# Performance work log

Measured on AMD Instinct MI355X. Metric: run time of the kernel, lower is better.

## Reference

```python
import jax, jax.numpy as jnp
import numpy as np

B, H, S, D_K = 4, 16, 2048, 64


def setup_inputs() -> dict:
    key = jax.random.key(0)
    kq, kk, kv = jax.random.split(key, 3)
    Q = jax.random.normal(kq, (B, H, S, D_K), dtype=jnp.float32)
    K = jax.random.normal(kk, (B, H, S, D_K), dtype=jnp.float32)
    V = jax.random.normal(kv, (B, H, S, D_K), dtype=jnp.float32)
    # causal mask: True = masked (matches torch masked_fill_ semantics)
    attn_mask = jnp.triu(jnp.ones((S, S), dtype=jnp.bool_), k=1)[None, None]
    return {"Q": Q, "K": K, "V": V, "attn_mask": attn_mask}


def reference(Q, K, V, attn_mask):
    d_k = Q.shape[-1]
    scale = 1.0 / np.sqrt(d_k).astype(np.float32)
    # scores: [B,H,S,S]
    scores = jnp.einsum("bhqd,bhkd->bhqk", Q, K) * scale
    scores = jnp.where(attn_mask, jnp.float32(-1e9), scores)
    attn = jax.nn.softmax(scores, axis=-1)
    context = jnp.einsum("bhqk,bhkd->bhqd", attn, V)
    return (context, attn)
```

## Files before the change

kernel.cpp:

```cpp
#include <hip/hip_runtime.h>


#define S 2048
#define DK 64
#define BH 64
#define NSTRIP 128
#define SCS 2056
#define VTS 2080
#define CTX_ELEMS (BH * S * DK)

typedef __attribute__((ext_vector_type(8))) short bf16x8;
typedef __attribute__((ext_vector_type(4))) float f32x4;

__device__ __forceinline__ short f2bf(float f) {
    union { float f; unsigned u; } v; v.f = f;
    unsigned r = (v.u + 0x7FFFu + ((v.u >> 16) & 1u)) >> 16;
    return (short)r;
}
__device__ __forceinline__ float bf2f(short s) {
    union { unsigned u; float f; } v;
    v.u = ((unsigned)(unsigned short)s) << 16;
    return v.f;
}
__device__ __forceinline__ bf16x8 pack8(float4 x, float4 y) {
    bf16x8 r;
    r[0] = f2bf(x.x); r[1] = f2bf(x.y); r[2] = f2bf(x.z); r[3] = f2bf(x.w);
    r[4] = f2bf(y.x); r[5] = f2bf(y.y); r[6] = f2bf(y.z); r[7] = f2bf(y.w);
    return r;
}

__global__ __launch_bounds__(256, 2)
void prepass_kernel(const float* __restrict__ K, const float* __restrict__ V,
                    short* __restrict__ Kbf, short* __restrict__ VT) {
    __shared__ short vt[64][72];
    const int bh = blockIdx.y;
    const int r0 = blockIdx.x * 64;
    const int tid = threadIdx.x;

    for (int u = tid; u < 512; u += 256) {
        const int row = u >> 3, col = (u & 7) * 8;
        const size_t off = ((size_t)(bh * S + r0 + row)) * DK + col;
        float4 x = *(const float4*)(K + off);
        float4 y = *(const float4*)(K + off + 4);
        *(bf16x8*)(Kbf + off) = pack8(x, y);
    }
    for (int u = tid; u < 512; u += 256) {
        const int row = u >> 3, col = (u & 7) * 8;
        const size_t off = ((size_t)(bh * S + r0 + row)) * DK + col;
        float4 x = *(const float4*)(V + off);
        float4 y = *(const float4*)(V + off + 4);
        bf16x8 p = pack8(x, y);
        #pragma unroll
        for (int j = 0; j < 8; ++j) vt[col + j][row] = p[j];
    }
    __syncthreads();
    {
        const int d = tid >> 2, seg = tid & 3;
        bf16x8 a = *(const bf16x8*)&vt[d][seg * 16];
        bf16x8 b = *(const bf16x8*)&vt[d][seg * 16 + 8];
        short* dst = VT + ((size_t)(bh * DK + d)) * VTS + r0 + seg * 16;
        *(bf16x8*)dst = a;
        *(bf16x8*)(dst + 8) = b;
    }
}

template<bool PRE>
__global__ __launch_bounds__(256, 2)
void sdpa_causal_kernel(const float* __restrict__ Q,
                        const float* __restrict__ K,
                        const float* __restrict__ V,
                        const short* __restrict__ Kbf,
                        const short* __restrict__ VT,
                        float* __restrict__ out) {
    __shared__ short sc[16 * SCS];
    __shared__ float row_inv[16];

    const int qb = NSTRIP - 1 - blockIdx.x;
    const int bh = blockIdx.y;
    const int qs = qb * 16;
    const int ncols = (qb + 1) * 16;

    const int tid = threadIdx.x;
    const int w = tid >> 6;
    const int lane = tid & 63;
    const int quad = lane >> 4;
    const int mrow = lane & 15;

    float* ctx  = out;
    float* attn = out + (size_t)CTX_ELEMS;

    {
        int4 z = {0, 0, 0, 0};
        int4* p = (int4*)sc;
        const int nchunks = (16 * SCS * 2) / 16;
        for (int i = tid; i < nchunks; i += 256) p[i] = z;
    }
    __syncthreads();

    {
        bf16x8 aQ[2];
        const float* Qrow = Q + ((size_t)(bh * S + qs + mrow)) * DK;
        #pragma unroll
        for (int kc = 0; kc < 2; ++kc) {
            float4 x = *(const float4*)(Qrow + kc * 32 + quad * 8);
            float4 y = *(const float4*)(Qrow + kc * 32 + quad * 8 + 4);
            aQ[kc] = pack8(x, y);
        }
        for (int nt = w; nt <= qb; nt += 4) {
            f32x4 acc = {0.f, 0.f, 0.f, 0.f};
            if (PRE) {
                const short* Krow = Kbf + ((size_t)(bh * S + nt * 16 + mrow)) * DK;
                bf16x8 bK0 = *(const bf16x8*)(Krow + quad * 8);
                bf16x8 bK1 = *(const bf16x8*)(Krow + 32 + quad * 8);
                acc = __builtin_amdgcn_mfma_f32_16x16x32_bf16(aQ[0], bK0, acc, 0, 0, 0);
                acc = __builtin_amdgcn_mfma_f32_16x16x32_bf16(aQ[1], bK1, acc, 0, 0, 0);
            } else {
                const float* Krow = K + ((size_t)(bh * S + nt * 16 + mrow)) * DK;
                #pragma unroll
                for (int kc = 0; kc < 2; ++kc) {
                    float4 x = *(const float4*)(Krow + kc * 32 + quad * 8);
                    float4 y = *(const float4*)(Krow + kc * 32 + quad * 8 + 4);
                    bf16x8 bK = pack8(x, y);
                    acc = __builtin_amdgcn_mfma_f32_16x16x32_bf16(aQ[kc], bK, acc, 0, 0, 0);
                }
            }
            #pragma unroll
            for (int r = 0; r < 4; ++r) {
                int rloc = quad * 4 + r;
                int gcol = nt * 16 + mrow;
                float val = acc[r] * 0.125f;
                if (gcol > qs + rloc) val = -INFINITY;
                sc[rloc * SCS + gcol] = f2bf(val);
            }
        }
    }
    __syncthreads();

    for (int r = 0; r < 4; ++r) {
        const int row = w * 4 + r;
        float mx = -INFINITY;
        for (int c = lane * 8; c < ncols; c += 512) {
            bf16x8 v = *(const bf16x8*)&sc[row * SCS + c];
            #pragma unroll
            for (int i = 0; i < 8; ++i) mx = fmaxf(mx, bf2f(v[i]));
        }
        #pragma unroll
        for (int off = 32; off; off >>= 1) mx = fmaxf(mx, __shfl_xor(mx, off));

        float sum = 0.f;
        for (int c = lane * 8; c < ncols; c += 512) {
            bf16x8 v = *(const bf16x8*)&sc[row * SCS + c];
            bf16x8 e;
            #pragma unroll
            for (int i = 0; i < 8; ++i) {
                float ev = __expf(bf2f(v[i]) - mx);
                sum += ev;
                e[i] = f2bf(ev);
            }
            *(bf16x8*)&sc[row * SCS + c] = e;
        }
        #pragma unroll
        for (int off = 32; off; off >>= 1) sum += __shfl_xor(sum, off);
        if (lane == 0) row_inv[row] = 1.0f / sum;
    }
    __syncthreads();

    {
        float* attnBase = attn + (size_t)(bh * S + qs) * S;
        const int c = tid * 8;
        for (int row = 0; row < 16; ++row) {
            float* dst = attnBase + (size_t)row * S + c;
            if (c < ncols) {
                const float invl = row_inv[row];
                bf16x8 v = *(const bf16x8*)&sc[row * SCS + c];
                float4 o0, o1;
                o0.x = bf2f(v[0]) * invl; o0.y = bf2f(v[1]) * invl;
                o0.z = bf2f(v[2]) * invl; o0.w = bf2f(v[3]) * invl;
                o1.x = bf2f(v[4]) * invl; o1.y = bf2f(v[5]) * invl;
                o1.z = bf2f(v[6]) * invl; o1.w = bf2f(v[7]) * invl;
                *(float4*)dst = o0;
                *(float4*)(dst + 4) = o1;
            } else {
                float4 z = {0.f, 0.f, 0.f, 0.f};
                *(float4*)dst = z;
                *(float4*)(dst + 4) = z;
            }
        }
    }

    f32x4 o0 = {0.f,0.f,0.f,0.f}, o1 = o0, o2 = o0, o3 = o0;
    {
        const int NC32 = (ncols + 31) >> 5;
        if (PRE) {
            const short* VTb = VT + (size_t)bh * DK * VTS;
            for (int c = w; c < NC32; c += 4) {
                const int j0 = c * 32;
                bf16x8 aP = *(const bf16x8*)&sc[mrow * SCS + j0 + quad * 8];
                #pragma unroll
                for (int dt = 0; dt < 4; ++dt) {
                    bf16x8 bV = *(const bf16x8*)&VTb[(size_t)(dt * 16 + mrow) * VTS + j0 + quad * 8];
                    f32x4 acc = dt == 0 ? o0 : dt == 1 ? o1 : dt == 2 ? o2 : o3;
                    acc = __builtin_amdgcn_mfma_f32_16x16x32_bf16(aP, bV, acc, 0, 0, 0);
                    if      (dt == 0) o0 = acc;
                    else if (dt == 1) o1 = acc;
                    else if (dt == 2) o2 = acc;
                    else              o3 = acc;
                }
            }
        } else {
            for (int c = w; c < NC32; c += 4) {
                const int j0 = c * 32;
                bf16x8 aP = *(const bf16x8*)&sc[mrow * SCS + j0 + quad * 8];
                #pragma unroll
                for (int dt = 0; dt < 4; ++dt) {
                    const float* Vp = V + ((size_t)(bh * S + j0 + quad * 8)) * DK + dt * 16 + mrow;
                    bf16x8 bV;
                    #pragma unroll
                    for (int jj = 0; jj < 8; ++jj) bV[jj] = f2bf(Vp[jj * DK]);
                    f32x4 acc = dt == 0 ? o0 : dt == 1 ? o1 : dt == 2 ? o2 : o3;
                    acc = __builtin_amdgcn_mfma_f32_16x16x32_bf16(aP, bV, acc, 0, 0, 0);
                    if      (dt == 0) o0 = acc;
                    else if (dt == 1) o1 = acc;
                    else if (dt == 2) o2 = acc;
                    else              o3 = acc;
                }
            }
        }
    }
    __syncthreads();

    {
        float* op = (float*)sc;
        #pragma unroll
        for (int dt = 0; dt < 4; ++dt) {
            f32x4 acc = dt == 0 ? o0 : dt == 1 ? o1 : dt == 2 ? o2 : o3;
            #pragma unroll
            for (int r = 0; r < 4; ++r)
                op[(w * 16 + quad * 4 + r) * 64 + dt * 16 + mrow] = acc[r];
        }
        __syncthreads();
        #pragma unroll
        for (int k = 0; k < 4; ++k) {
            int idx = tid + k * 256;
            int row = idx >> 6, d = idx & 63;
            float s = op[row * 64 + d] + op[(16 + row) * 64 + d]
                    + op[(32 + row) * 64 + d] + op[(48 + row) * 64 + d];
            ctx[((size_t)(bh * S + qs + row)) * DK + d] = s * row_inv[row];
        }
    }
}

extern "C" void kernel_launch(void* const* d_in, const int* in_sizes, int n_in,
                              void* d_out, int out_size, void* d_ws, size_t ws_size,
                              hipStream_t stream) {
    const float* Q = (const float*)d_in[0];
    const float* K = (const float*)d_in[1];
    const float* V = (const float*)d_in[2];
    float* out = (float*)d_out;
    dim3 grid(NSTRIP, BH);

    const size_t kbf_bytes = (size_t)BH * S * DK * sizeof(short);
    const size_t vt_bytes  = (size_t)BH * DK * VTS * sizeof(short);
    if (ws_size >= kbf_bytes + vt_bytes) {
        short* Kbf = (short*)d_ws;
        short* VT  = (short*)((char*)d_ws + kbf_bytes);
        prepass_kernel<<<dim3(S / 64, BH), 256, 0, stream>>>(K, V, Kbf, VT);
        sdpa_causal_kernel<true><<<grid, 256, 0, stream>>>(Q, K, V, Kbf, VT, out);
    } else {
        sdpa_causal_kernel<false><<<grid, 256, 0, stream>>>(Q, K, V, nullptr, nullptr, out);
    }
}
```

Measured before the change: 1.506 ms.

## Replace full score-strip LDS buffer with two-pass online-softmax streaming kernel

The main path no longer materializes a 16x2048 bf16 score strip in shared memory. A first pass computes the QK^T tiles and keeps a per-row online max and sum in registers, merged across waves. A second pass recomputes the scores, writes the normalized attention straight to global memory, and feeds a small per-wave LDS tile into the PV MFMA. Cutting LDS use allows four blocks per CU, and block IDs are swizzled to interleave heads; the cost is computing QK^T twice.

```diff
diff --git a/kernel.cpp b/kernel.cpp
--- a/kernel.cpp
+++ b/kernel.cpp
@@ -5,11 +5,12 @@
 #define DK 64
 #define BH 64
 #define NSTRIP 128
-#define SCS 2056
 #define VTS 2080
+#define ELD 40
 #define CTX_ELEMS (BH * S * DK)
 
 typedef __attribute__((ext_vector_type(8))) short bf16x8;
+typedef __attribute__((ext_vector_type(4))) short bf16x4;
 typedef __attribute__((ext_vector_type(4))) float f32x4;
 
 __device__ __forceinline__ short f2bf(float f) {
@@ -64,39 +65,183 @@
     }
 }
 
-template<bool PRE>
+__global__ __launch_bounds__(256, 4)
+void sdpa_causal_main(const float* __restrict__ Q,
+                      const short* __restrict__ Kbf,
+                      const short* __restrict__ VT,
+                      float* __restrict__ out) {
+    __shared__ short elds[4][16][ELD];
+    __shared__ float stats_m[4][16];
+    __shared__ float stats_l[4][16];
+    __shared__ float row_inv[16];
+    __shared__ float osum[4][16][64];
+
+    const int id = blockIdx.y * NSTRIP + blockIdx.x;
+    const int sw = (id & 7) * (NSTRIP * BH / 8) + (id >> 3);
+    const int bh = sw >> 7;
+    const int qb = NSTRIP - 1 - (sw & 127);
+    const int qs = qb * 16;
+    const int ncols = (qb + 1) * 16;
+
+    const int tid = threadIdx.x;
+    const int w = tid >> 6, lane = tid & 63;
+    const int quad = lane >> 4, mrow = lane & 15;
+    const int qrow = qs + mrow;
+
+    float* ctx  = out;
+    float* attn = out + (size_t)CTX_ELEMS;
+
+    bf16x8 bQ0, bQ1;
+    {
+        const float* Qrow = Q + ((size_t)(bh * S + qrow)) * DK;
+        float4 x0 = *(const float4*)(Qrow + quad * 8);
+        float4 y0 = *(const float4*)(Qrow + quad * 8 + 4);
+        bQ0 = pack8(x0, y0);
+        float4 x1 = *(const float4*)(Qrow + 32 + quad * 8);
+        float4 y1 = *(const float4*)(Qrow + 32 + quad * 8 + 4);
+        bQ1 = pack8(x1, y1);
+    }
+
+    float m0 = -1e30f, l0 = 0.f;
+    for (int nt = w; nt <= qb; nt += 4) {
+        const short* Krow = Kbf + ((size_t)(bh * S + nt * 16 + mrow)) * DK;
+        bf16x8 aK0 = *(const bf16x8*)(Krow + quad * 8);
+        bf16x8 aK1 = *(const bf16x8*)(Krow + 32 + quad * 8);
+        f32x4 acc = {0.f, 0.f, 0.f, 0.f};
+        acc = __builtin_amdgcn_mfma_f32_16x16x32_bf16(aK0, bQ0, acc, 0, 0, 0);
+        acc = __builtin_amdgcn_mfma_f32_16x16x32_bf16(aK1, bQ1, acc, 0, 0, 0);
+        const int keyb = nt * 16 + quad * 4;
+        float s0 = (keyb + 0 <= qrow) ? acc[0] * 0.125f : -1e30f;
+        float s1 = (keyb + 1 <= qrow) ? acc[1] * 0.125f : -1e30f;
+        float s2 = (keyb + 2 <= qrow) ? acc[2] * 0.125f : -1e30f;
+        float s3 = (keyb + 3 <= qrow) ? acc[3] * 0.125f : -1e30f;
+        float t = fmaxf(fmaxf(s0, s1), fmaxf(s2, s3));
+        float mn = fmaxf(m0, t);
+        l0 = l0 * __expf(m0 - mn)
+           + __expf(s0 - mn) + __expf(s1 - mn)
+           + __expf(s2 - mn) + __expf(s3 - mn);
+        m0 = mn;
+    }
+    #pragma unroll
+    for (int off = 16; off <= 32; off <<= 1) {
+        float m2 = __shfl_xor(m0, off);
+        float l2 = __shfl_xor(l0, off);
+        float mg = fmaxf(m0, m2);
+        l0 = l0 * __expf(m0 - mg) + l2 * __expf(m2 - mg);
+        m0 = mg;
+    }
+    if (lane < 16) { stats_m[w][lane] = m0; stats_l[w][lane] = l0; }
+
+    {
+        float* base = attn + (size_t)(bh * S + qs) * S;
+        const float4 z = {0.f, 0.f, 0.f, 0.f};
+        for (int row = 0; row < 16; ++row)
+            for (int c = ncols + tid * 4; c < S; c += 1024)
+                *(float4*)(base + (size_t)row * S + c) = z;
+    }
+    __syncthreads();
+
+    float mF = stats_m[0][mrow], lF = stats_l[0][mrow];
+    #pragma unroll
+    for (int ww = 1; ww < 4; ++ww) {
+        float m2 = stats_m[ww][mrow], l2 = stats_l[ww][mrow];
+        float mg = fmaxf(mF, m2);
+        lF = lF * __expf(mF - mg) + l2 * __expf(m2 - mg);
+        mF = mg;
+    }
+    const float invl = 1.f / lF;
+    if (w == 0 && lane < 16) row_inv[lane] = invl;
+
+    f32x4 o0 = {0.f,0.f,0.f,0.f}, o1 = o0, o2 = o0, o3 = o0;
+    short* erow = &elds[w][mrow][0];
+    const short* VTb = VT + (size_t)bh * DK * VTS;
+    float* attnRow = attn + ((size_t)(bh * S + qrow)) * S;
+    const int npair = (qb + 2) >> 1;
+    for (int pp = w; pp < npair; pp += 4) {
+        #pragma unroll
+        for (int half = 0; half < 2; ++half) {
+            const int nt = 2 * pp + half;
+            if (nt <= qb) {
+                const short* Krow = Kbf + ((size_t)(bh * S + nt * 16 + mrow)) * DK;
+                bf16x8 aK0 = *(const bf16x8*)(Krow + quad * 8);
+                bf16x8 aK1 = *(const bf16x8*)(Krow + 32 + quad * 8);
+                f32x4 acc = {0.f, 0.f, 0.f, 0.f};
+                acc = __builtin_amdgcn_mfma_f32_16x16x32_bf16(aK0, bQ0, acc, 0, 0, 0);
+                acc = __builtin_amdgcn_mfma_f32_16x16x32_bf16(aK1, bQ1, acc, 0, 0, 0);
+                const int keyb = nt * 16 + quad * 4;
+                float e0, e1, e2, e3;
+                {
+                    float sv;
+                    sv = (keyb + 0 <= qrow) ? acc[0] * 0.125f : -1e30f; e0 = __expf(sv - mF);
+                    sv = (keyb + 1 <= qrow) ? acc[1] * 0.125f : -1e30f; e1 = __expf(sv - mF);
+                    sv = (keyb + 2 <= qrow) ? acc[2] * 0.125f : -1e30f; e2 = __expf(sv - mF);
+                    sv = (keyb + 3 <= qrow) ? acc[3] * 0.125f : -1e30f; e3 = __expf(sv - mF);
+                }
+                float4 av;
+                av.x = e0 * invl; av.y = e1 * invl;
+                av.z = e2 * invl; av.w = e3 * invl;
+                *(float4*)(attnRow + keyb) = av;
+                bf16x4 eb;
+                eb[0] = f2bf(e0); eb[1] = f2bf(e1);
+                eb[2] = f2bf(e2); eb[3] = f2bf(e3);
+                *(bf16x4*)(erow + half * 16 + quad * 4) = eb;
+            } else {
+                bf16x4 zb = {0, 0, 0, 0};
+                *(bf16x4*)(erow + half * 16 + quad * 4) = zb;
+            }
+        }
+        bf16x8 aP = *(const bf16x8*)&elds[w][mrow][quad * 8];
+        const size_t vco = (size_t)pp * 32 + quad * 8;
+        #pragma unroll
+        for (int dt = 0; dt < 4; ++dt) {
+            bf16x8 bV = *(const bf16x8*)(VTb + (size_t)(dt * 16 + mrow) * VTS + vco);
+            f32x4 a = dt == 0 ? o0 : dt == 1 ? o1 : dt == 2 ? o2 : o3;
+            a = __builtin_amdgcn_mfma_f32_16x16x32_bf16(aP, bV, a, 0, 0, 0);
+            if      (dt == 0) o0 = a;
+            else if (dt == 1) o1 = a;
+            else if (dt == 2) o2 = a;
+            else              o3 = a;
+        }
+    }
+
+    #pragma unroll
+    for (int dt = 0; dt < 4; ++dt) {
+        f32x4 a = dt == 0 ? o0 : dt == 1 ? o1 : dt == 2 ? o2 : o3;
+        #pragma unroll
+        for (int r = 0; r < 4; ++r)
+            osum[w][quad * 4 + r][dt * 16 + mrow] = a[r];
+    }
+    __syncthreads();
+    #pragma unroll
+    for (int k = 0; k < 4; ++k) {
+        int idx = tid + k * 256;
+        int row = idx >> 6, d = idx & 63;
+        float sv = osum[0][row][d] + osum[1][row][d]
+                 + osum[2][row][d] + osum[3][row][d];
+        ctx[((size_t)(bh * S + qs + row)) * DK + d] = sv * row_inv[row];
+    }
+}
+
 __global__ __launch_bounds__(256, 2)
-void sdpa_causal_kernel(const float* __restrict__ Q,
-                        const float* __restrict__ K,
-                        const float* __restrict__ V,
-                        const short* __restrict__ Kbf,
-                        const short* __restrict__ VT,
-                        float* __restrict__ out) {
-    __shared__ short sc[16 * SCS];
+void sdpa_causal_fb(const float* __restrict__ Q, const float* __restrict__ K,
+                    const float* __restrict__ V, float* __restrict__ out) {
+    __shared__ short sc[16 * 2056];
     __shared__ float row_inv[16];
-
     const int qb = NSTRIP - 1 - blockIdx.x;
     const int bh = blockIdx.y;
     const int qs = qb * 16;
     const int ncols = (qb + 1) * 16;
-
     const int tid = threadIdx.x;
-    const int w = tid >> 6;
-    const int lane = tid & 63;
-    const int quad = lane >> 4;
-    const int mrow = lane & 15;
-
+    const int w = tid >> 6, lane = tid & 63;
+    const int quad = lane >> 4, mrow = lane & 15;
     float* ctx  = out;
     float* attn = out + (size_t)CTX_ELEMS;
-
-    {
-        int4 z = {0, 0, 0, 0};
+    {
+        int4 z = {0,0,0,0};
         int4* p = (int4*)sc;
-        const int nchunks = (16 * SCS * 2) / 16;
-        for (int i = tid; i < nchunks; i += 256) p[i] = z;
-    }
-    __syncthreads();
-
+        for (int i = tid; i < (16 * 2056 * 2) / 16; i += 256) p[i] = z;
+    }
+    __syncthreads();
     {
         bf16x8 aQ[2];
         const float* Qrow = Q + ((size_t)(bh * S + qs + mrow)) * DK;
@@ -107,22 +252,14 @@
             aQ[kc] = pack8(x, y);
         }
         for (int nt = w; nt <= qb; nt += 4) {
-            f32x4 acc = {0.f, 0.f, 0.f, 0.f};
-            if (PRE) {
-                const short* Krow = Kbf + ((size_t)(bh * S + nt * 16 + mrow)) * DK;
-                bf16x8 bK0 = *(const bf16x8*)(Krow + quad * 8);
-                bf16x8 bK1 = *(const bf16x8*)(Krow + 32 + quad * 8);
-                acc = __builtin_amdgcn_mfma_f32_16x16x32_bf16(aQ[0], bK0, acc, 0, 0, 0);
-                acc = __builtin_amdgcn_mfma_f32_16x16x32_bf16(aQ[1], bK1, acc, 0, 0, 0);
-            } else {
-                const float* Krow = K + ((size_t)(bh * S + nt * 16 + mrow)) * DK;
-                #pragma unroll
-                for (int kc = 0; kc < 2; ++kc) {
-                    float4 x = *(const float4*)(Krow + kc * 32 + quad * 8);
-                    float4 y = *(const float4*)(Krow + kc * 32 + quad * 8 + 4);
-                    bf16x8 bK = pack8(x, y);
-                    acc = __builtin_amdgcn_mfma_f32_16x16x32_bf16(aQ[kc], bK, acc, 0, 0, 0);
-                }
+            const float* Krow = K + ((size_t)(bh * S + nt * 16 + mrow)) * DK;
+            f32x4 acc = {0.f,0.f,0.f,0.f};
+            #pragma unroll
+            for (int kc = 0; kc < 2; ++kc) {
+                float4 x = *(const float4*)(Krow + kc * 32 + quad * 8);
+                float4 y = *(const float4*)(Krow + kc * 32 + quad * 8 + 4);
+                bf16x8 bK = pack8(x, y);
+                acc = __builtin_amdgcn_mfma_f32_16x16x32_bf16(aQ[kc], bK, acc, 0, 0, 0);
             }
             #pragma unroll
             for (int r = 0; r < 4; ++r) {
@@ -130,41 +267,37 @@
                 int gcol = nt * 16 + mrow;
                 float val = acc[r] * 0.125f;
                 if (gcol > qs + rloc) val = -INFINITY;
-                sc[rloc * SCS + gcol] = f2bf(val);
-            }
-        }
-    }
-    __syncthreads();
-
+                sc[rloc * 2056 + gcol] = f2bf(val);
+            }
+        }
+    }
+    __syncthreads();
     for (int r = 0; r < 4; ++r) {
         const int row = w * 4 + r;
         float mx = -INFINITY;
         for (int c = lane * 8; c < ncols; c += 512) {
-            bf16x8 v = *(const bf16x8*)&sc[row * SCS + c];
+            bf16x8 v = *(const bf16x8*)&sc[row * 2056 + c];
             #pragma unroll
             for (int i = 0; i < 8; ++i) mx = fmaxf(mx, bf2f(v[i]));
         }
         #pragma unroll
         for (int off = 32; off; off >>= 1) mx = fmaxf(mx, __shfl_xor(mx, off));
-
         float sum = 0.f;
         for (int c = lane * 8; c < ncols; c += 512) {
-            bf16x8 v = *(const bf16x8*)&sc[row * SCS + c];
+            bf16x8 v = *(const bf16x8*)&sc[row * 2056 + c];
             bf16x8 e;
             #pragma unroll
             for (int i = 0; i < 8; ++i) {
                 float ev = __expf(bf2f(v[i]) - mx);
-                sum += ev;
-                e[i] = f2bf(ev);
-            }
-            *(bf16x8*)&sc[row * SCS + c] = e;
+                sum += ev; e[i] = f2bf(ev);
+            }
+            *(bf16x8*)&sc[row * 2056 + c] = e;
         }
         #pragma unroll
         for (int off = 32; off; off >>= 1) sum += __shfl_xor(sum, off);
         if (lane == 0) row_inv[row] = 1.0f / sum;
     }
     __syncthreads();
-
     {
         float* attnBase = attn + (size_t)(bh * S + qs) * S;
         const int c = tid * 8;
@@ -172,71 +305,49 @@
             float* dst = attnBase + (size_t)row * S + c;
             if (c < ncols) {
                 const float invl = row_inv[row];
-                bf16x8 v = *(const bf16x8*)&sc[row * SCS + c];
-                float4 o0, o1;
-                o0.x = bf2f(v[0]) * invl; o0.y = bf2f(v[1]) * invl;
-                o0.z = bf2f(v[2]) * invl; o0.w = bf2f(v[3]) * invl;
-                o1.x = bf2f(v[4]) * invl; o1.y = bf2f(v[5]) * invl;
-                o1.z = bf2f(v[6]) * invl; o1.w = bf2f(v[7]) * invl;
-                *(float4*)dst = o0;
-                *(float4*)(dst + 4) = o1;
+                bf16x8 v = *(const bf16x8*)&sc[row * 2056 + c];
+                float4 a0, a1;
+                a0.x = bf2f(v[0]) * invl; a0.y = bf2f(v[1]) * invl;
+                a0.z = bf2f(v[2]) * invl; a0.w = bf2f(v[3]) * invl;
+                a1.x = bf2f(v[4]) * invl; a1.y = bf2f(v[5]) * invl;
+                a1.z = bf2f(v[6]) * invl; a1.w = bf2f(v[7]) * invl;
+                *(float4*)dst = a0; *(float4*)(dst + 4) = a1;
             } else {
-                float4 z = {0.f, 0.f, 0.f, 0.f};
-                *(float4*)dst = z;
-                *(float4*)(dst + 4) = z;
-            }
-        }
-    }
-
+                float4 z = {0.f,0.f,0.f,0.f};
+                *(float4*)dst = z; *(float4*)(dst + 4) = z;
+            }
+        }
+    }
     f32x4 o0 = {0.f,0.f,0.f,0.f}, o1 = o0, o2 = o0, o3 = o0;
     {
         const int NC32 = (ncols + 31) >> 5;
-        if (PRE) {
-            const short* VTb = VT + (size_t)bh * DK * VTS;
-            for (int c = w; c < NC32; c += 4) {
-                const int j0 = c * 32;
-                bf16x8 aP = *(const bf16x8*)&sc[mrow * SCS + j0 + quad * 8];
+        for (int c = w; c < NC32; c += 4) {
+            const int j0 = c * 32;
+            bf16x8 aP = *(const bf16x8*)&sc[mrow * 2056 + j0 + quad * 8];
+            #pragma unroll
+            for (int dt = 0; dt < 4; ++dt) {
+                const float* Vp = V + ((size_t)(bh * S + j0 + quad * 8)) * DK + dt * 16 + mrow;
+                bf16x8 bV;
                 #pragma unroll
-                for (int dt = 0; dt < 4; ++dt) {
-                    bf16x8 bV = *(const bf16x8*)&VTb[(size_t)(dt * 16 + mrow) * VTS + j0 + quad * 8];
-                    f32x4 acc = dt == 0 ? o0 : dt == 1 ? o1 : dt == 2 ? o2 : o3;
-                    acc = __builtin_amdgcn_mfma_f32_16x16x32_bf16(aP, bV, acc, 0, 0, 0);
-                    if      (dt == 0) o0 = acc;
-                    else if (dt == 1) o1 = acc;
-                    else if (dt == 2) o2 = acc;
-                    else              o3 = acc;
-                }
-            }
-        } else {
-            for (int c = w; c < NC32; c += 4) {
-                const int j0 = c * 32;
-                bf16x8 aP = *(const bf16x8*)&sc[mrow * SCS + j0 + quad * 8];
-                #pragma unroll
-                for (int dt = 0; dt < 4; ++dt) {
-                    const float* Vp = V + ((size_t)(bh * S + j0 + quad * 8)) * DK + dt * 16 + mrow;
-                    bf16x8 bV;
-                    #pragma unroll
-                    for (int jj = 0; jj < 8; ++jj) bV[jj] = f2bf(Vp[jj * DK]);
-                    f32x4 acc = dt == 0 ? o0 : dt == 1 ? o1 : dt == 2 ? o2 : o3;
-                    acc = __builtin_amdgcn_mfma_f32_16x16x32_bf16(aP, bV, acc, 0, 0, 0);
-                    if      (dt == 0) o0 = acc;
-                    else if (dt == 1) o1 = acc;
-                    else if (dt == 2) o2 = acc;
-                    else              o3 = acc;
-                }
-            }
-        }
-    }
-    __syncthreads();
-
+                for (int jj = 0; jj < 8; ++jj) bV[jj] = f2bf(Vp[jj * DK]);
+                f32x4 a = dt == 0 ? o0 : dt == 1 ? o1 : dt == 2 ? o2 : o3;
+                a = __builtin_amdgcn_mfma_f32_16x16x32_bf16(aP, bV, a, 0, 0, 0);
+                if      (dt == 0) o0 = a;
+                else if (dt == 1) o1 = a;
+                else if (dt == 2) o2 = a;
+                else              o3 = a;
+            }
+        }
+    }
+    __syncthreads();
     {
         float* op = (float*)sc;
         #pragma unroll
         for (int dt = 0; dt < 4; ++dt) {
-            f32x4 acc = dt == 0 ? o0 : dt == 1 ? o1 : dt == 2 ? o2 : o3;
+            f32x4 a = dt == 0 ? o0 : dt == 1 ? o1 : dt == 2 ? o2 : o3;
             #pragma unroll
             for (int r = 0; r < 4; ++r)
-                op[(w * 16 + quad * 4 + r) * 64 + dt * 16 + mrow] = acc[r];
+                op[(w * 16 + quad * 4 + r) * 64 + dt * 16 + mrow] = a[r];
         }
         __syncthreads();
         #pragma unroll
@@ -265,8 +376,8 @@
         short* Kbf = (short*)d_ws;
         short* VT  = (short*)((char*)d_ws + kbf_bytes);
         prepass_kernel<<<dim3(S / 64, BH), 256, 0, stream>>>(K, V, Kbf, VT);
-        sdpa_causal_kernel<true><<<grid, 256, 0, stream>>>(Q, K, V, Kbf, VT, out);
+        sdpa_causal_main<<<grid, 256, 0, stream>>>(Q, Kbf, VT, out);
     } else {
-        sdpa_causal_kernel<false><<<grid, 256, 0, stream>>>(Q, K, V, nullptr, nullptr, out);
-    }
-}
+        sdpa_causal_fb<<<grid, 256, 0, stream>>>(Q, K, V, out);
+    }
+}
```

New measurement: 1.452 ms. 1.04x faster.
